# Optimization experiments

Measured on AMD Instinct MI355X. Metric: run time of the kernel, lower is better.

The kernel has to match this reference:

```python
import jax, jax.numpy as jnp
import numpy as np

B, S, D = 4, 256, 2048
E, F, K = 32, 768, 8


def setup_inputs() -> dict:
    key = jax.random.key(0)
    k1, k2, k3, k4, k5 = jax.random.split(key, 5)
    sc_in = 1.0 / np.sqrt(D)
    sc_f = 1.0 / np.sqrt(F)
    return {
        "hidden_states": jax.random.normal(k1, (B, S, D), jnp.float32),
        "gate_w": jax.random.normal(k2, (E, D), jnp.float32) * sc_in,   # nn.Linear(D, E).weight
        "wg": jax.random.normal(k3, (E, F, D), jnp.float32) * sc_in,    # gate_proj weights [E, F, D]
        "wu": jax.random.normal(k4, (E, F, D), jnp.float32) * sc_in,    # up_proj weights   [E, F, D]
        "wd": jax.random.normal(k5, (E, D, F), jnp.float32) * sc_f,     # down_proj weights [E, D, F]
    }


def reference(hidden_states, gate_w, wg, wu, wd):
    b, s, d = hidden_states.shape
    x = hidden_states.reshape(-1, d)                        # [T, D]
    T = x.shape[0]

    # Router: linear -> softmax over experts -> top-k -> renormalize
    router_logits = jnp.einsum("td,ed->te", x, gate_w)      # [T, E]
    routing_probs = jax.nn.softmax(router_logits, axis=-1)
    topk_w, topk_idx = jax.lax.top_k(routing_probs, K)      # [T, K]
    topk_w = topk_w / jnp.sum(topk_w, axis=-1, keepdims=True)  # norm_topk_prob=True

    # Scatter top-k weights to dense [T, E] combine weights (zeros for unselected experts)
    combine = jnp.zeros((T, wg.shape[0]), x.dtype).at[
        jnp.arange(T)[:, None], topk_idx
    ].set(topk_w)                                           # [T, E]

    # Expert gated MLPs (computed for all experts, combined with sparse weights)
    g = jnp.einsum("td,efd->etf", x, wg)                    # [E, T, F]
    u = jnp.einsum("td,efd->etf", x, wu)                    # [E, T, F]
    h = jax.nn.silu(g) * u                                  # [E, T, F]
    y = jnp.einsum("etf,edf->etd", h, wd)                   # [E, T, D]

    out = jnp.einsum("te,etd->td", combine, y)              # [T, D]
    return out.reshape(b, s, d)
```

## Files before the change

kernel.cpp:

```cpp
#include <hip/hip_runtime.h>

#define T_TOK 1024
#define D_DIM 2048
#define E_NUM 32
#define F_DIM 768
#define K_TOP 8

typedef __bf16 v8bf __attribute__((ext_vector_type(8)));
typedef float v4f __attribute__((ext_vector_type(4)));
typedef unsigned short v8us __attribute__((ext_vector_type(8)));

__device__ __forceinline__ unsigned short f2b(float f) {
  unsigned int u = __builtin_bit_cast(unsigned int, f);
  u += 0x7fffu + ((u >> 16) & 1u);
  return (unsigned short)(u >> 16);
}
__device__ __forceinline__ float b2f(unsigned short s) {
  return __builtin_bit_cast(float, (unsigned int)s << 16);
}
__device__ __forceinline__ v8us cvt8u(v4f a, v4f b) {
  v8bf r;
  r[0] = (__bf16)a[0]; r[1] = (__bf16)a[1]; r[2] = (__bf16)a[2]; r[3] = (__bf16)a[3];
  r[4] = (__bf16)b[0]; r[5] = (__bf16)b[1]; r[6] = (__bf16)b[2]; r[7] = (__bf16)b[3];
  return __builtin_bit_cast(v8us, r);
}
__device__ __forceinline__ void gload16(const void* g, void* l) {
  __builtin_amdgcn_global_load_lds(
      (const __attribute__((address_space(1))) void*)g,
      (__attribute__((address_space(3))) void*)l, 16, 0, 0);
}
__device__ __forceinline__ v4f gload4f(const char* p) {
  v4f r;
  asm volatile("global_load_dwordx4 %0, %1, off" : "=v"(r) : "v"(p));
  return r;
}

#define VMWAIT(N) asm volatile("s_waitcnt vmcnt(" #N ")" ::: "memory")
#define LGKM0() asm volatile("s_waitcnt lgkmcnt(0)" ::: "memory")
#define SBAR() __builtin_amdgcn_s_barrier()
#define SCHEDB() __builtin_amdgcn_sched_barrier(0)

__global__ __launch_bounds__(256) void router_kernel(
    const float* __restrict__ x, const float* __restrict__ gw,
    unsigned short* __restrict__ xb, int* __restrict__ counts,
    int* __restrict__ tlist, int* __restrict__ topk_e, int* __restrict__ topk_p,
    float* __restrict__ topk_w, float* __restrict__ wlist)
{
  const int t = blockIdx.x, tid = threadIdx.x;
  const float* xr = x + (size_t)t * D_DIM;

  {
    v4f f0 = *reinterpret_cast<const v4f*>(xr + tid * 8);
    v4f f1 = *reinterpret_cast<const v4f*>(xr + tid * 8 + 4);
    *reinterpret_cast<v8us*>(xb + (size_t)t * D_DIM + tid * 8) = cvt8u(f0, f1);
  }

  __shared__ float logits[E_NUM];
  const int lane = tid & 63, wave = tid >> 6;
  for (int j = 0; j < 8; ++j) {
    int e = wave * 8 + j;
    const float* wr = gw + (size_t)e * D_DIM;
    float s = 0.f;
#pragma unroll
    for (int i = 0; i < D_DIM / 64; ++i) s = fmaf(xr[lane + i * 64], wr[lane + i * 64], s);
#pragma unroll
    for (int off = 32; off > 0; off >>= 1) s += __shfl_xor(s, off);
    if (lane == 0) logits[e] = s;
  }
  __syncthreads();

  if (tid == 0) {
    float lg[E_NUM];
#pragma unroll
    for (int e2 = 0; e2 < E_NUM; ++e2) lg[e2] = logits[e2];
    int sel[K_TOP]; float sv[K_TOP];
    for (int k = 0; k < K_TOP; ++k) {
      int best = 0; float bv = -3.4e38f;
      for (int e2 = 0; e2 < E_NUM; ++e2)
        if (lg[e2] > bv) { bv = lg[e2]; best = e2; }
      sel[k] = best; sv[k] = bv; lg[best] = -3.4e38f;
    }
    float mx = sv[0], s8 = 0.f, ww[K_TOP];
    for (int k = 0; k < K_TOP; ++k) { ww[k] = __expf(sv[k] - mx); s8 += ww[k]; }
    float inv = 1.f / s8;
    for (int k = 0; k < K_TOP; ++k) {
      float w = ww[k] * inv;
      int e2 = sel[k];
      int pos = atomicAdd(&counts[e2], 1);
      tlist[e2 * T_TOK + pos] = t;
      wlist[e2 * T_TOK + pos] = w;
      topk_e[t * K_TOP + k] = e2;
      topk_p[t * K_TOP + k] = pos;
      topk_w[t * K_TOP + k] = w;
    }
  }
}

__global__ void scan_kernel(const int* __restrict__ counts, int* __restrict__ offsets)
{
  if (threadIdx.x == 0) {
    int run = 0;
    for (int e = 0; e < E_NUM; ++e) { offsets[e] = run; run += counts[e]; }
  }
}

__global__ __launch_bounds__(512, 4) void gateup_kernel(
    const unsigned short* __restrict__ xb, const float* __restrict__ wg,
    const float* __restrict__ wu, const int* __restrict__ counts,
    const int* __restrict__ offsets, const int* __restrict__ tlist,
    unsigned short* __restrict__ hbuf)
{
  const int bid = blockIdx.x;
  const int xcd = bid & 7;
  const int j = bid >> 3;
  const int e = xcd + 8 * (j / 24);
  const int r = j % 24;
  const int tf = r >> 1;
  const int tm = r & 1;
  const int cnt = counts[e];
  if (tm * 192 >= cnt) return;

  __shared__ __align__(16) unsigned char lds[81920];

  const int tid = threadIdx.x;
  const int lane = tid & 63;
  const int wave = tid >> 6;
  const int wm = wave >> 1;
  const int wn = wave & 1;
  const int l15 = lane & 15;
  const int l4 = lane >> 4;

  const char* xbB = (const char*)xb;
  unsigned asrc[3], adst[3];
#pragma unroll
  for (int c = 0; c < 3; ++c) {
    int idx = tid + c * 512;
    int rr = idx >> 3, gl = idx & 7;
    int rg = tm * 192 + rr;
    if (rg > cnt - 1) rg = cnt - 1;
    int tok = tlist[e * T_TOK + rg];
    int gg = gl ^ (rr & 7);
    asrc[c] = (unsigned)tok * 4096u + (unsigned)(gg * 16);
    adst[c] = (unsigned)(idx * 16);
  }
  const int brow = tid >> 3, bg8 = tid & 7;
  const unsigned bsrc = (unsigned)((tf * 64 + brow) * 8192 + bg8 * 32);
  const unsigned bdst = (unsigned)(brow * 128 + ((bg8 ^ (brow & 7)) * 16));
  const char* gB = (const char*)wg + (size_t)e * F_DIM * D_DIM * 4;
  const char* uB = (const char*)wu + (size_t)e * F_DIM * D_DIM * 4;

  unsigned aRd[3];
#pragma unroll
  for (int fm = 0; fm < 3; ++fm) {
    int row = wm * 48 + fm * 16 + l15;
    aRd[fm] = (unsigned)(row * 128 + ((l4 ^ (row & 7)) * 16));
  }
  unsigned bRd[2];
#pragma unroll
  for (int fn = 0; fn < 2; ++fn) {
    int row = wn * 32 + fn * 16 + l15;
    bRd[fn] = (unsigned)(row * 128 + ((l4 ^ (row & 7)) * 16));
  }

  v4f zero = {0.f, 0.f, 0.f, 0.f};
  v4f accg[3][2], accu[3][2];
#pragma unroll
  for (int fm = 0; fm < 3; ++fm)
#pragma unroll
    for (int fn = 0; fn < 2; ++fn) { accg[fm][fn] = zero; accu[fm][fn] = zero; }

  auto COMPUTE = [&](unsigned ab, unsigned bb, unsigned sx) {
    v8bf af[3], bg[2], bu[2];
#pragma unroll
    for (int fm = 0; fm < 3; ++fm)
      af[fm] = __builtin_bit_cast(v8bf,
          *reinterpret_cast<const v8us*>(&lds[ab + (aRd[fm] ^ sx)]));
#pragma unroll
    for (int fn = 0; fn < 2; ++fn) {
      bg[fn] = __builtin_bit_cast(v8bf,
          *reinterpret_cast<const v8us*>(&lds[bb + (bRd[fn] ^ sx)]));
      bu[fn] = __builtin_bit_cast(v8bf,
          *reinterpret_cast<const v8us*>(&lds[bb + 8192u + (bRd[fn] ^ sx)]));
    }
#pragma unroll
    for (int fm = 0; fm < 3; ++fm)
#pragma unroll
      for (int fn = 0; fn < 2; ++fn) {
        accg[fm][fn] = __builtin_amdgcn_mfma_f32_16x16x32_bf16(af[fm], bg[fn], accg[fm][fn], 0, 0, 0);
        accu[fm][fn] = __builtin_amdgcn_mfma_f32_16x16x32_bf16(af[fm], bu[fn], accu[fm][fn], 0, 0, 0);
      }
  };

  const int NG = D_DIM / 64;

  v4f g0 = gload4f(gB + bsrc);
  v4f g1 = gload4f(gB + bsrc + 16);
  v4f u0 = gload4f(uB + bsrc);
  v4f u1 = gload4f(uB + bsrc + 16);
  SCHEDB();
#pragma unroll
  for (int c = 0; c < 3; ++c) gload16(xbB + asrc[c], &lds[adst[c]]);
  SCHEDB();

#pragma unroll 2
  for (int i = 0; i < NG; ++i) {
    const unsigned ab = (unsigned)(i & 1) * 24576u;
    const unsigned bb = 49152u + (unsigned)(i & 1) * 16384u;
    VMWAIT(3); SCHEDB();
    *reinterpret_cast<v8us*>(&lds[bb + bdst]) = cvt8u(g0, g1);
    *reinterpret_cast<v8us*>(&lds[bb + 8192u + bdst]) = cvt8u(u0, u1);
    if (i + 1 < NG) {
      const unsigned an = (unsigned)((i + 1) & 1) * 24576u;
      unsigned bo = bsrc + (unsigned)(i + 1) * 256u;
      g0 = gload4f(gB + bo);
      g1 = gload4f(gB + bo + 16);
      u0 = gload4f(uB + bo);
      u1 = gload4f(uB + bo + 16);
      SCHEDB();
      unsigned ao = (unsigned)(i + 1) * 128u;
#pragma unroll
      for (int c = 0; c < 3; ++c) gload16(xbB + asrc[c] + ao, &lds[an + adst[c]]);
      SCHEDB();
      VMWAIT(7);
    } else {
      VMWAIT(0);
    }
    SCHEDB(); LGKM0(); SBAR(); SCHEDB();
    COMPUTE(ab, bb, 0u);
    COMPUTE(ab, bb, 64u);
    SCHEDB(); SBAR();
  }

  const int off_e = offsets[e];
#pragma unroll
  for (int fm = 0; fm < 3; ++fm)
#pragma unroll
    for (int fn = 0; fn < 2; ++fn)
#pragma unroll
      for (int i = 0; i < 4; ++i) {
        int rloc = wm * 48 + fm * 16 + l4 * 4 + i;
        int rg = tm * 192 + rloc;
        if (rg < cnt) {
          int col = tf * 64 + wn * 32 + fn * 16 + l15;
          float g = accg[fm][fn][i];
          float uu = accu[fm][fn][i];
          float h = g * (1.f / (1.f + __expf(-g))) * uu;
          hbuf[(size_t)(off_e + rg) * F_DIM + col] = f2b(h);
        }
      }
}

template <int STAGEOUT>
__global__ __launch_bounds__(512, 4) void down_kernel(
    const unsigned short* __restrict__ hbuf, const float* __restrict__ wd,
    const int* __restrict__ counts, const int* __restrict__ offsets,
    const int* __restrict__ tlist, const float* __restrict__ wlist,
    unsigned short* __restrict__ ybuf, float* __restrict__ out)
{
  const int bid = blockIdx.x;
  const int xcd = bid & 7;
  const int j = bid >> 3;
  const int e = xcd + 8 * (j / 64);
  const int r = j % 64;
  const int td = r >> 1;
  const int tm = r & 1;
  const int cnt = counts[e];
  if (tm * 192 >= cnt) return;
  const int off_e = offsets[e];

  __shared__ __align__(16) unsigned char lds[65536];

  const int tid = threadIdx.x;
  const int lane = tid & 63;
  const int wave = tid >> 6;
  const int wm = wave >> 1;
  const int wn = wave & 1;
  const int l15 = lane & 15;
  const int l4 = lane >> 4;

  const char* hB = (const char*)hbuf;
  unsigned asrc[3], adst[3];
#pragma unroll
  for (int c = 0; c < 3; ++c) {
    int idx = tid + c * 512;
    int rr = idx >> 3, gl = idx & 7;
    int rg = tm * 192 + rr;
    if (rg > cnt - 1) rg = cnt - 1;
    int gg = gl ^ (rr & 7);
    asrc[c] = (unsigned)(off_e + rg) * 1536u + (unsigned)(gg * 16);
    adst[c] = (unsigned)(idx * 16);
  }
  const int brow = tid >> 3, bg8 = tid & 7;
  const unsigned bsrc = (unsigned)((td * 64 + brow) * 3072 + bg8 * 32);
  const unsigned bdst = (unsigned)(brow * 128 + ((bg8 ^ (brow & 7)) * 16));
  const char* bB = (const char*)wd + (size_t)e * D_DIM * F_DIM * 4;

  unsigned aRd[3];
#pragma unroll
  for (int fm = 0; fm < 3; ++fm) {
    int row = wm * 48 + fm * 16 + l15;
    aRd[fm] = (unsigned)(row * 128 + ((l4 ^ (row & 7)) * 16));
  }
  unsigned bRd[2];
#pragma unroll
  for (int fn = 0; fn < 2; ++fn) {
    int row = wn * 32 + fn * 16 + l15;
    bRd[fn] = (unsigned)(row * 128 + ((l4 ^ (row & 7)) * 16));
  }

  v4f zero = {0.f, 0.f, 0.f, 0.f};
  v4f acc[3][2];
#pragma unroll
  for (int fm = 0; fm < 3; ++fm)
#pragma unroll
    for (int fn = 0; fn < 2; ++fn) acc[fm][fn] = zero;

  auto COMPUTE = [&](unsigned ab, unsigned bb, unsigned sx) {
    v8bf af[3], bf_[2];
#pragma unroll
    for (int fm = 0; fm < 3; ++fm)
      af[fm] = __builtin_bit_cast(v8bf,
          *reinterpret_cast<const v8us*>(&lds[ab + (aRd[fm] ^ sx)]));
#pragma unroll
    for (int fn = 0; fn < 2; ++fn)
      bf_[fn] = __builtin_bit_cast(v8bf,
          *reinterpret_cast<const v8us*>(&lds[bb + (bRd[fn] ^ sx)]));
#pragma unroll
    for (int fm = 0; fm < 3; ++fm)
#pragma unroll
      for (int fn = 0; fn < 2; ++fn)
        acc[fm][fn] = __builtin_amdgcn_mfma_f32_16x16x32_bf16(af[fm], bf_[fn], acc[fm][fn], 0, 0, 0);
  };

  const int NG = F_DIM / 64;

  v4f b0 = gload4f(bB + bsrc);
  v4f b1 = gload4f(bB + bsrc + 16);
  SCHEDB();
#pragma unroll
  for (int c = 0; c < 3; ++c) gload16(hB + asrc[c], &lds[adst[c]]);
  SCHEDB();

#pragma unroll 2
  for (int i = 0; i < NG; ++i) {
    const unsigned ab = (unsigned)(i & 1) * 24576u;
    const unsigned bb = 49152u + (unsigned)(i & 1) * 8192u;
    VMWAIT(3); SCHEDB();
    *reinterpret_cast<v8us*>(&lds[bb + bdst]) = cvt8u(b0, b1);
    if (i + 1 < NG) {
      const unsigned an = (unsigned)((i + 1) & 1) * 24576u;
      unsigned bo = bsrc + (unsigned)(i + 1) * 256u;
      b0 = gload4f(bB + bo);
      b1 = gload4f(bB + bo + 16);
      SCHEDB();
      unsigned ao = (unsigned)(i + 1) * 128u;
#pragma unroll
      for (int c = 0; c < 3; ++c) gload16(hB + asrc[c] + ao, &lds[an + adst[c]]);
      SCHEDB();
      VMWAIT(5);
    } else {
      VMWAIT(0);
    }
    SCHEDB(); LGKM0(); SBAR(); SCHEDB();
    COMPUTE(ab, bb, 0u);
    COMPUTE(ab, bb, 64u);
    SCHEDB(); SBAR();
  }

#pragma unroll
  for (int fm = 0; fm < 3; ++fm)
#pragma unroll
    for (int fn = 0; fn < 2; ++fn)
#pragma unroll
      for (int i = 0; i < 4; ++i) {
        int rloc = wm * 48 + fm * 16 + l4 * 4 + i;
        int rg = tm * 192 + rloc;
        if (rg < cnt) {
          int col = td * 64 + wn * 32 + fn * 16 + l15;
          float y = acc[fm][fn][i];
          if (STAGEOUT) {
            ybuf[(size_t)(off_e + rg) * D_DIM + col] = f2b(y);
          } else {
            int tok = tlist[e * T_TOK + rg];
            float w = wlist[e * T_TOK + rg];
            atomicAdd(out + (size_t)tok * D_DIM + col, w * y);
          }
        }
      }
}

__global__ __launch_bounds__(256) void combine_kernel(
    const unsigned short* __restrict__ ybuf, const int* __restrict__ topk_e,
    const int* __restrict__ topk_p, const float* __restrict__ topk_w,
    const int* __restrict__ offsets, float* __restrict__ out)
{
  const int t = blockIdx.x, tid = threadIdx.x;
  const int d0 = tid * 8;
  float acc[8] = {0.f, 0.f, 0.f, 0.f, 0.f, 0.f, 0.f, 0.f};
#pragma unroll
  for (int k = 0; k < K_TOP; ++k) {
    int e = topk_e[t * K_TOP + k];
    int slot = offsets[e] + topk_p[t * K_TOP + k];
    float w = topk_w[t * K_TOP + k];
    v8us v = *reinterpret_cast<const v8us*>(ybuf + (size_t)slot * D_DIM + d0);
#pragma unroll
    for (int j = 0; j < 8; ++j) acc[j] += w * b2f(v[j]);
  }
  v4f o0 = {acc[0], acc[1], acc[2], acc[3]};
  v4f o1 = {acc[4], acc[5], acc[6], acc[7]};
  *reinterpret_cast<v4f*>(out + (size_t)t * D_DIM + d0) = o0;
  *reinterpret_cast<v4f*>(out + (size_t)t * D_DIM + d0 + 4) = o1;
}

extern "C" void kernel_launch(void* const* d_in, const int* in_sizes, int n_in,
                              void* d_out, int out_size, void* d_ws, size_t ws_size,
                              hipStream_t stream)
{
  const float* x  = (const float*)d_in[0];
  const float* gw = (const float*)d_in[1];
  const float* wg = (const float*)d_in[2];
  const float* wu = (const float*)d_in[3];
  const float* wd = (const float*)d_in[4];
  float* out = (float*)d_out;

  char* p = (char*)d_ws;
  auto alloc = [&](size_t bytes) {
    char* r = p;
    p += (bytes + 255) & ~(size_t)255;
    return r;
  };
  int* counts   = (int*)alloc(E_NUM * 4);
  int* offsets  = (int*)alloc(E_NUM * 4);
  int* tlist    = (int*)alloc((size_t)E_NUM * T_TOK * 4);
  float* wlist  = (float*)alloc((size_t)E_NUM * T_TOK * 4);
  int* topk_e   = (int*)alloc((size_t)T_TOK * K_TOP * 4);
  int* topk_p   = (int*)alloc((size_t)T_TOK * K_TOP * 4);
  float* topk_w = (float*)alloc((size_t)T_TOK * K_TOP * 4);
  unsigned short* xb   = (unsigned short*)alloc((size_t)T_TOK * D_DIM * 2);
  unsigned short* hbuf = (unsigned short*)alloc((size_t)T_TOK * K_TOP * F_DIM * 2);
  size_t need_atomic = (size_t)(p - (char*)d_ws);
  unsigned short* ybuf = (unsigned short*)alloc((size_t)T_TOK * K_TOP * D_DIM * 2);
  size_t need_stage = (size_t)(p - (char*)d_ws);

  if (ws_size < need_atomic) return;
  const bool stage = (ws_size >= need_stage);

  hipMemsetAsync(counts, 0, E_NUM * 4, stream);
  router_kernel<<<T_TOK, 256, 0, stream>>>(x, gw, xb, counts, tlist, topk_e, topk_p, topk_w, wlist);
  scan_kernel<<<1, 64, 0, stream>>>(counts, offsets);
  gateup_kernel<<<dim3(24 * E_NUM), 512, 0, stream>>>(
      xb, wg, wu, counts, offsets, tlist, hbuf);
  if (stage) {
    down_kernel<1><<<dim3(64 * E_NUM), 512, 0, stream>>>(
        hbuf, wd, counts, offsets, tlist, wlist, ybuf, out);
    combine_kernel<<<T_TOK, 256, 0, stream>>>(ybuf, topk_e, topk_p, topk_w, offsets, out);
  } else {
    hipMemsetAsync(out, 0, (size_t)out_size * 4, stream);
    down_kernel<0><<<dim3(64 * E_NUM), 512, 0, stream>>>(
        hbuf, wd, counts, offsets, tlist, wlist, ybuf, out);
  }
}
```

Before: 267.3 us.

## Widen down-proj tile to 128 output columns and raise MFMA wave priority

The down-projection kernel now covers 128 D-columns per block instead of 64, halving the grid. Each wave holds a 3x4 accumulator tile, and the B tile in LDS is doubled so each A tile of hbuf loaded into LDS is reused over twice as many columns. Both kernels also raise wave priority around the MFMA compute section using s_setprio. In exchange, each block needs 80 KB of LDS and more registers, which lowers occupancy, and the smaller grid gives the GPU fewer blocks to spread across its compute units.

```diff
diff --git a/kernel.cpp b/kernel.cpp
--- a/kernel.cpp
+++ b/kernel.cpp
@@ -226,8 +226,10 @@
       VMWAIT(0);
     }
     SCHEDB(); LGKM0(); SBAR(); SCHEDB();
+    __builtin_amdgcn_s_setprio(1);
     COMPUTE(ab, bb, 0u);
     COMPUTE(ab, bb, 64u);
+    __builtin_amdgcn_s_setprio(0);
     SCHEDB(); SBAR();
   }
 
@@ -260,15 +262,15 @@
   const int bid = blockIdx.x;
   const int xcd = bid & 7;
   const int j = bid >> 3;
-  const int e = xcd + 8 * (j / 64);
-  const int r = j % 64;
+  const int e = xcd + 8 * (j / 32);
+  const int r = j % 32;
   const int td = r >> 1;
   const int tm = r & 1;
   const int cnt = counts[e];
   if (tm * 192 >= cnt) return;
   const int off_e = offsets[e];
 
-  __shared__ __align__(16) unsigned char lds[65536];
+  __shared__ __align__(16) unsigned char lds[81920];
 
   const int tid = threadIdx.x;
   const int lane = tid & 63;
@@ -290,10 +292,16 @@
     asrc[c] = (unsigned)(off_e + rg) * 1536u + (unsigned)(gg * 16);
     adst[c] = (unsigned)(idx * 16);
   }
-  const int brow = tid >> 3, bg8 = tid & 7;
-  const unsigned bsrc = (unsigned)((td * 64 + brow) * 3072 + bg8 * 32);
-  const unsigned bdst = (unsigned)(brow * 128 + ((bg8 ^ (brow & 7)) * 16));
   const char* bB = (const char*)wd + (size_t)e * D_DIM * F_DIM * 4;
+  const char* bp[2];
+  unsigned bdst[2];
+#pragma unroll
+  for (int c = 0; c < 2; ++c) {
+    int idx = tid + c * 512;
+    int row = idx >> 3, pr = idx & 7;
+    bp[c] = bB + (size_t)(td * 128 + row) * 3072 + pr * 32;
+    bdst[c] = (unsigned)(row * 128 + ((pr ^ (row & 7)) * 16));
+  }
 
   unsigned aRd[3];
 #pragma unroll
@@ -301,41 +309,42 @@
     int row = wm * 48 + fm * 16 + l15;
     aRd[fm] = (unsigned)(row * 128 + ((l4 ^ (row & 7)) * 16));
   }
-  unsigned bRd[2];
-#pragma unroll
-  for (int fn = 0; fn < 2; ++fn) {
-    int row = wn * 32 + fn * 16 + l15;
+  unsigned bRd[4];
+#pragma unroll
+  for (int fn = 0; fn < 4; ++fn) {
+    int row = wn * 64 + fn * 16 + l15;
     bRd[fn] = (unsigned)(row * 128 + ((l4 ^ (row & 7)) * 16));
   }
 
   v4f zero = {0.f, 0.f, 0.f, 0.f};
-  v4f acc[3][2];
+  v4f acc[3][4];
 #pragma unroll
   for (int fm = 0; fm < 3; ++fm)
 #pragma unroll
-    for (int fn = 0; fn < 2; ++fn) acc[fm][fn] = zero;
+    for (int fn = 0; fn < 4; ++fn) acc[fm][fn] = zero;
 
   auto COMPUTE = [&](unsigned ab, unsigned bb, unsigned sx) {
-    v8bf af[3], bf_[2];
+    v8bf af[3], bf_[4];
 #pragma unroll
     for (int fm = 0; fm < 3; ++fm)
       af[fm] = __builtin_bit_cast(v8bf,
           *reinterpret_cast<const v8us*>(&lds[ab + (aRd[fm] ^ sx)]));
 #pragma unroll
-    for (int fn = 0; fn < 2; ++fn)
+    for (int fn = 0; fn < 4; ++fn)
       bf_[fn] = __builtin_bit_cast(v8bf,
           *reinterpret_cast<const v8us*>(&lds[bb + (bRd[fn] ^ sx)]));
 #pragma unroll
     for (int fm = 0; fm < 3; ++fm)
 #pragma unroll
-      for (int fn = 0; fn < 2; ++fn)
+      for (int fn = 0; fn < 4; ++fn)
         acc[fm][fn] = __builtin_amdgcn_mfma_f32_16x16x32_bf16(af[fm], bf_[fn], acc[fm][fn], 0, 0, 0);
   };
 
   const int NG = F_DIM / 64;
 
-  v4f b0 = gload4f(bB + bsrc);
-  v4f b1 = gload4f(bB + bsrc + 16);
+  v4f b0[2], b1[2];
+#pragma unroll
+  for (int c = 0; c < 2; ++c) { b0[c] = gload4f(bp[c]); b1[c] = gload4f(bp[c] + 16); }
   SCHEDB();
 #pragma unroll
   for (int c = 0; c < 3; ++c) gload16(hB + asrc[c], &lds[adst[c]]);
@@ -344,39 +353,43 @@
 #pragma unroll 2
   for (int i = 0; i < NG; ++i) {
     const unsigned ab = (unsigned)(i & 1) * 24576u;
-    const unsigned bb = 49152u + (unsigned)(i & 1) * 8192u;
+    const unsigned bb = 49152u + (unsigned)(i & 1) * 16384u;
     VMWAIT(3); SCHEDB();
-    *reinterpret_cast<v8us*>(&lds[bb + bdst]) = cvt8u(b0, b1);
+#pragma unroll
+    for (int c = 0; c < 2; ++c)
+      *reinterpret_cast<v8us*>(&lds[bb + bdst[c]]) = cvt8u(b0[c], b1[c]);
     if (i + 1 < NG) {
       const unsigned an = (unsigned)((i + 1) & 1) * 24576u;
-      unsigned bo = bsrc + (unsigned)(i + 1) * 256u;
-      b0 = gload4f(bB + bo);
-      b1 = gload4f(bB + bo + 16);
+      const unsigned ko = (unsigned)(i + 1) * 256u;
+#pragma unroll
+      for (int c = 0; c < 2; ++c) { b0[c] = gload4f(bp[c] + ko); b1[c] = gload4f(bp[c] + ko + 16); }
       SCHEDB();
-      unsigned ao = (unsigned)(i + 1) * 128u;
+      const unsigned ao = (unsigned)(i + 1) * 128u;
 #pragma unroll
       for (int c = 0; c < 3; ++c) gload16(hB + asrc[c] + ao, &lds[an + adst[c]]);
       SCHEDB();
-      VMWAIT(5);
+      VMWAIT(7);
     } else {
       VMWAIT(0);
     }
     SCHEDB(); LGKM0(); SBAR(); SCHEDB();
+    __builtin_amdgcn_s_setprio(1);
     COMPUTE(ab, bb, 0u);
     COMPUTE(ab, bb, 64u);
+    __builtin_amdgcn_s_setprio(0);
     SCHEDB(); SBAR();
   }
 
 #pragma unroll
   for (int fm = 0; fm < 3; ++fm)
 #pragma unroll
-    for (int fn = 0; fn < 2; ++fn)
+    for (int fn = 0; fn < 4; ++fn)
 #pragma unroll
       for (int i = 0; i < 4; ++i) {
         int rloc = wm * 48 + fm * 16 + l4 * 4 + i;
         int rg = tm * 192 + rloc;
         if (rg < cnt) {
-          int col = td * 64 + wn * 32 + fn * 16 + l15;
+          int col = td * 128 + wn * 64 + fn * 16 + l15;
           float y = acc[fm][fn][i];
           if (STAGEOUT) {
             ybuf[(size_t)(off_e + rg) * D_DIM + col] = f2b(y);
@@ -451,12 +464,12 @@
   gateup_kernel<<<dim3(24 * E_NUM), 512, 0, stream>>>(
       xb, wg, wu, counts, offsets, tlist, hbuf);
   if (stage) {
-    down_kernel<1><<<dim3(64 * E_NUM), 512, 0, stream>>>(
+    down_kernel<1><<<dim3(32 * E_NUM), 512, 0, stream>>>(
         hbuf, wd, counts, offsets, tlist, wlist, ybuf, out);
     combine_kernel<<<T_TOK, 256, 0, stream>>>(ybuf, topk_e, topk_p, topk_w, offsets, out);
   } else {
     hipMemsetAsync(out, 0, (size_t)out_size * 4, stream);
-    down_kernel<0><<<dim3(64 * E_NUM), 512, 0, stream>>>(
+    down_kernel<0><<<dim3(32 * E_NUM), 512, 0, stream>>>(
         hbuf, wd, counts, offsets, tlist, wlist, ybuf, out);
   }
 }
```

New measurement: 310.3 us. 16.1% more time.
